# Performance work log

Measured on AMD Instinct MI355X. Metric: run time of the kernel, lower is better.

## Reference

```python
import jax, jax.numpy as jnp
import numpy as np

D_PROJ = 256
SCALE = D_PROJ ** (-0.5)


def setup_inputs() -> dict:
    key = jax.random.key(0)
    k1, k2, k3, k4 = jax.random.split(key, 4)
    B, L, Dh = 16, 2048, 1280
    T, Dg = 512, 768
    H = jax.random.normal(k1, (B, L, Dh), dtype=jnp.float32)
    G = jax.random.normal(k2, (B, T, Dg), dtype=jnp.float32)
    # Linear weights (torch nn.Linear: out = x @ W.T), small init to keep softmax well-conditioned
    Wq = jax.random.normal(k3, (D_PROJ, Dg), dtype=jnp.float32) * 0.02
    Wk = jax.random.normal(k4, (D_PROJ, Dh), dtype=jnp.float32) * 0.02
    return {"H": H, "G": G, "Wq": Wq, "Wk": Wk}


def reference(H, G, Wq, Wk):
    # Q = Wq(G): [B,T,P]; K = Wk(H): [B,L,P]
    Q = jnp.einsum('btg,pg->btp', G, Wq)
    K = jnp.einsum('bld,pd->blp', H, Wk)
    # The torch module's chunked online-softmax computes exact softmax over L.
    logits = jnp.einsum('btp,blp->btl', Q, K) * SCALE  # [B,T,L]
    A = jax.nn.softmax(logits, axis=-1)
    # Values are the raw residue embeddings H (not projected).
    Z = jnp.einsum('btl,bld->btd', A, H)  # [B,T,Dh]
    return Z
```

## Files before the change

### kernel.cpp

```cpp
#include <hip/hip_runtime.h>
#include <stdint.h>

typedef __attribute__((ext_vector_type(8))) short   short8;
typedef __attribute__((ext_vector_type(8))) __bf16  bf16x8;
typedef __attribute__((ext_vector_type(4))) float   floatx4;

#define DEV static __device__ __forceinline__

DEV unsigned short f2b(float f) {
  union { float f; unsigned u; } v; v.f = f;
  unsigned u = v.u;
  unsigned r = u + 0x7FFFu + ((u >> 16) & 1u);
  return (unsigned short)(r >> 16);
}

DEV void gload_lds16(const void* g, void* l) {
  __builtin_amdgcn_global_load_lds(
      (const __attribute__((address_space(1))) unsigned int*)g,
      (__attribute__((address_space(3))) unsigned int*)l,
      16, 0, 0);
}

__global__ void cvtw_kernel(const float* __restrict__ a, unsigned short* __restrict__ oa, int na4,
                            const float* __restrict__ b, unsigned short* __restrict__ ob, int nb4,
                            float* __restrict__ zp, int nz) {
  int i = blockIdx.x * blockDim.x + threadIdx.x;
  if (i < na4) {
    float4 v = ((const float4*)a)[i];
    ushort4 o; o.x = f2b(v.x); o.y = f2b(v.y); o.z = f2b(v.z); o.w = f2b(v.w);
    ((ushort4*)oa)[i] = o;
  } else if (i < na4 + nb4) {
    int k = i - na4;
    float4 v = ((const float4*)b)[k];
    ushort4 o; o.x = f2b(v.x); o.y = f2b(v.y); o.z = f2b(v.z); o.w = f2b(v.w);
    ((ushort4*)ob)[k] = o;
  } else if (i < na4 + nb4 + nz) {
    zp[i - na4 - nb4] = 0.f;
  }
}

template <int WRITE_HT>
__global__ __launch_bounds__(256) void proj_gemm(
    const float* __restrict__ A32, const unsigned short* __restrict__ Bt,
    unsigned short* __restrict__ C, unsigned short* __restrict__ HT,
    int K, int lda) {
  __shared__ float          Af32[2][64 * 32];
  __shared__ unsigned short Bs[2][256 * 32];
  __shared__ unsigned short As[64 * 32];
  __shared__ unsigned short At2[WRITE_HT ? 32 * 66 : 1];

  const int m0   = blockIdx.x * 64;
  const int t    = threadIdx.x;
  const int lane = t & 63;
  const int wave = t >> 6;
  const int wn   = wave * 64;
  const int r16  = lane & 15;
  const int q    = lane >> 4;
  const int nt   = K >> 5;

  floatx4 acc[4][4];
#pragma unroll
  for (int i = 0; i < 4; ++i)
#pragma unroll
    for (int j = 0; j < 4; ++j) acc[i][j] = (floatx4){0.f, 0.f, 0.f, 0.f};

  auto stage = [&](int it, int buf) {
    const int kt = it << 5;
#pragma unroll
    for (int cc = 0; cc < 2; ++cc) {
      int c = t + cc * 256;
      gload_lds16(A32 + (size_t)(m0 + (c >> 3)) * lda + kt + (c & 7) * 4,
                  &Af32[buf][c * 4]);
    }
#pragma unroll
    for (int cc = 0; cc < 4; ++cc) {
      int c = t + cc * 256;
      gload_lds16(Bt + (size_t)(c >> 2) * K + kt + (c & 3) * 8, &Bs[buf][c * 8]);
    }
  };

  stage(0, 0);
  stage(1, 1);

  for (int it = 0; it < nt; ++it) {
    const int cur = it & 1;
    const int kt  = it << 5;

    if (it == nt - 1) { asm volatile("s_waitcnt vmcnt(0)" ::: "memory"); }
    else              { asm volatile("s_waitcnt vmcnt(6)" ::: "memory"); }
    __builtin_amdgcn_sched_barrier(0);

    {
      const int row = t >> 3;
      const int kc  = t & 7;
      float4 v0 = *(const float4*)&Af32[cur][t * 4];
      float4 v1 = *(const float4*)&Af32[cur][t * 4 + 1024];
      unsigned short e0[4], e1[4];
      e0[0] = f2b(v0.x); e0[1] = f2b(v0.y); e0[2] = f2b(v0.z); e0[3] = f2b(v0.w);
      e1[0] = f2b(v1.x); e1[1] = f2b(v1.y); e1[2] = f2b(v1.z); e1[3] = f2b(v1.w);
      ushort4 p0, p1;
      p0.x = e0[0]; p0.y = e0[1]; p0.z = e0[2]; p0.w = e0[3];
      p1.x = e1[0]; p1.y = e1[1]; p1.z = e1[2]; p1.w = e1[3];
      *(ushort4*)&As[row * 32 + kc * 4]        = p0;
      *(ushort4*)&As[(row + 32) * 32 + kc * 4] = p1;
      if constexpr (WRITE_HT) {
#pragma unroll
        for (int jj = 0; jj < 4; ++jj) {
          At2[(kc * 4 + jj) * 66 + row]      = e0[jj];
          At2[(kc * 4 + jj) * 66 + row + 32] = e1[jj];
        }
      }
    }
    asm volatile("s_waitcnt lgkmcnt(0)\n\ts_barrier" ::: "memory");
    __builtin_amdgcn_sched_barrier(0);

    bf16x8 af[4], bfr[4];
#pragma unroll
    for (int i = 0; i < 4; ++i) af[i]  = *(const bf16x8*)&As[(i * 16 + r16) * 32 + q * 8];
#pragma unroll
    for (int j = 0; j < 4; ++j) bfr[j] = *(const bf16x8*)&Bs[cur][(wn + j * 16 + r16) * 32 + q * 8];
    union { unsigned u[4]; short8 s; } vv;
    if constexpr (WRITE_HT) {
      const int d  = t >> 3;
      const int lc = t & 7;
      const unsigned* w = (const unsigned*)At2 + d * 33 + lc * 4;
      vv.u[0] = w[0]; vv.u[1] = w[1]; vv.u[2] = w[2]; vv.u[3] = w[3];
    }
    asm volatile("s_waitcnt lgkmcnt(0)\n\ts_barrier" ::: "memory");
    __builtin_amdgcn_sched_barrier(0);

    if (it + 2 < nt) stage(it + 2, cur);

#pragma unroll
    for (int i = 0; i < 4; ++i)
#pragma unroll
      for (int j = 0; j < 4; ++j)
        acc[i][j] = __builtin_amdgcn_mfma_f32_16x16x32_bf16(af[i], bfr[j], acc[i][j], 0, 0, 0);

    if constexpr (WRITE_HT) {
      const int d  = t >> 3;
      const int lc = t & 7;
      const int b  = m0 >> 11;
      const int l0 = m0 & 2047;
      *(short8*)&HT[((size_t)b * 1280 + kt + d) * 2048 + l0 + lc * 8] = vv.s;
    }
  }

#pragma unroll
  for (int i = 0; i < 4; ++i) {
#pragma unroll
    for (int r = 0; r < 4; ++r) {
      int m = m0 + i * 16 + q * 4 + r;
#pragma unroll
      for (int j = 0; j < 4; ++j) {
        int n = wn + j * 16 + r16;
        C[(size_t)m * 256 + n] = f2b(acc[i][j][r]);
      }
    }
  }
}

template <int EPI>
__global__ void gemm_nt(const unsigned short* __restrict__ Ab, const unsigned short* __restrict__ Btb,
                        void* __restrict__ Cpv, float* __restrict__ sums,
                        int K, int lda, int ldb, int ldc,
                        long long sA, long long sB, long long sC, int sstride,
                        float escale, int nx, int tiles_pb) {
  __shared__ unsigned short As[128 * 32];
  __shared__ unsigned short Bs[128 * 32];

  const int g   = blockIdx.x;
  const int xcd = g & 7;
  const int jj  = g >> 3;
  const int bz  = xcd * 2 + jj / tiles_pb;
  const int tt  = jj % tiles_pb;
  const int m0  = (tt / nx) * 128;
  const int n0  = (tt % nx) * 128;

  const int t    = threadIdx.x;
  const int lane = t & 63;
  const int wave = t >> 6;
  const int wm   = (wave & 1) * 64;
  const int wn   = (wave >> 1) * 64;
  const int r16  = lane & 15;
  const int q    = lane >> 4;

  const unsigned short* Bt = Btb + (long long)bz * sB;
  const unsigned short* A  = Ab + (long long)bz * sA;

  floatx4 acc[4][4];
#pragma unroll
  for (int i = 0; i < 4; ++i)
#pragma unroll
    for (int j = 0; j < 4; ++j) acc[i][j] = (floatx4){0.f, 0.f, 0.f, 0.f};

  for (int kt = 0; kt < K; kt += 32) {
    __syncthreads();
#pragma unroll
    for (int cc = 0; cc < 2; ++cc) {
      int c = t + cc * 256;
      gload_lds16(Bt + (size_t)(n0 + (c >> 2)) * ldb + kt + (c & 3) * 8, &Bs[c * 8]);
    }
#pragma unroll
    for (int cc = 0; cc < 2; ++cc) {
      int c = t + cc * 256;
      gload_lds16(A + (size_t)(m0 + (c >> 2)) * lda + kt + (c & 3) * 8, &As[c * 8]);
    }
    __syncthreads();

    bf16x8 af[4], bfr[4];
#pragma unroll
    for (int i = 0; i < 4; ++i) af[i]  = *(const bf16x8*)&As[(wm + i * 16 + r16) * 32 + q * 8];
#pragma unroll
    for (int j = 0; j < 4; ++j) bfr[j] = *(const bf16x8*)&Bs[(wn + j * 16 + r16) * 32 + q * 8];
#pragma unroll
    for (int i = 0; i < 4; ++i)
#pragma unroll
      for (int j = 0; j < 4; ++j)
        acc[i][j] = __builtin_amdgcn_mfma_f32_16x16x32_bf16(af[i], bfr[j], acc[i][j], 0, 0, 0);
  }

  if constexpr (EPI == 1) {
    unsigned short* C = (unsigned short*)Cpv + (long long)bz * sC;
#pragma unroll
    for (int i = 0; i < 4; ++i) {
#pragma unroll
      for (int r = 0; r < 4; ++r) {
        int m = m0 + wm + i * 16 + q * 4 + r;
        float ps = 0.f;
#pragma unroll
        for (int j = 0; j < 4; ++j) {
          int n = n0 + wn + j * 16 + r16;
          float v = __expf(acc[i][j][r] * escale);
          ps += v;
          C[(size_t)m * ldc + n] = f2b(v);
        }
#pragma unroll
        for (int msk = 1; msk < 16; msk <<= 1) ps += __shfl_xor(ps, msk, 64);
        if (r16 == 0) atomicAdd(&sums[(long long)bz * sstride + m], ps);
      }
    }
  } else {
    float* C = (float*)Cpv + (long long)bz * sC;
    const float* sb = sums + (long long)bz * sstride;
#pragma unroll
    for (int i = 0; i < 4; ++i) {
#pragma unroll
      for (int r = 0; r < 4; ++r) {
        int m = m0 + wm + i * 16 + q * 4 + r;
        float sc = 1.0f / sb[m];
#pragma unroll
        for (int j = 0; j < 4; ++j) {
          int n = n0 + wn + j * 16 + r16;
          C[(size_t)m * ldc + n] = acc[i][j][r] * sc;
        }
      }
    }
  }
}

extern "C" void kernel_launch(void* const* d_in, const int* in_sizes, int n_in,
                              void* d_out, int out_size, void* d_ws, size_t ws_size,
                              hipStream_t stream) {
  (void)in_sizes; (void)n_in; (void)out_size; (void)ws_size;
  const float* H  = (const float*)d_in[0];
  const float* G  = (const float*)d_in[1];
  const float* Wq = (const float*)d_in[2];
  const float* Wk = (const float*)d_in[3];
  float* Z = (float*)d_out;

  constexpr int B = 16, L = 2048, Dh = 1280, T = 512, Dg = 768, P = 256;

  char* ws = (char*)d_ws;
  size_t off = 0;
  auto alloc = [&](size_t bytes) { void* p = ws + off; off += (bytes + 255) & ~(size_t)255; return p; };
  unsigned short* Wqbf = (unsigned short*)alloc((size_t)P * Dg * 2);
  unsigned short* Wkbf = (unsigned short*)alloc((size_t)P * Dh * 2);
  unsigned short* Qbf  = (unsigned short*)alloc((size_t)B * T * P * 2);
  unsigned short* Kbf  = (unsigned short*)alloc((size_t)B * L * P * 2);
  unsigned short* HT   = (unsigned short*)alloc((size_t)B * Dh * L * 2);
  unsigned short* E    = (unsigned short*)alloc((size_t)B * T * L * 2);
  float*          sums = (float*)alloc((size_t)B * T * 4);

  {
    int na4 = P * Dg / 4, nb4 = P * Dh / 4, nz = B * T;
    cvtw_kernel<<<(na4 + nb4 + nz + 255) / 256, 256, 0, stream>>>(
        Wq, Wqbf, na4, Wk, Wkbf, nb4, sums, nz);
  }

  proj_gemm<0><<<B * T / 64, 256, 0, stream>>>(G, Wqbf, Qbf, nullptr, Dg, Dg);
  proj_gemm<1><<<B * L / 64, 256, 0, stream>>>(H, Wkbf, Kbf, HT, Dh, Dh);

  gemm_nt<1><<<B * (T / 128) * (L / 128), 256, 0, stream>>>(
      Qbf, Kbf, E, sums, P, P, P, L,
      (long long)T * P, (long long)L * P, (long long)T * L, T,
      0.0625f, L / 128, (T / 128) * (L / 128));

  gemm_nt<2><<<B * (T / 128) * (Dh / 128), 256, 0, stream>>>(
      E, HT, Z, sums, L, L, L, Dh,
      (long long)T * L, (long long)Dh * L, (long long)T * Dh, T,
      0.f, Dh / 128, (T / 128) * (Dh / 128));
}
```

Baseline: 410.9 us.

## Add dedicated 128-row K projection kernel with register-staged fp32 loads

Replaces the templated K projection, which also writes the bf16 transpose of H, with a new proj_k kernel using 128-row tiles and 512 threads (2x4 wave grid). The fp32 H tile is now loaded into registers and converted there instead of being staged through LDS with global_load_lds. The loop is unrolled by two with explicit vmcnt bookkeeping, and each staged W tile is shared by twice as many rows. This is meant to cut LDS traffic and per-row weight reloads in the largest projection, at the cost of more registers and a bigger block.

```diff
diff --git a/kernel.cpp b/kernel.cpp
--- a/kernel.cpp
+++ b/kernel.cpp
@@ -47,7 +47,6 @@
   __shared__ float          Af32[2][64 * 32];
   __shared__ unsigned short Bs[2][256 * 32];
   __shared__ unsigned short As[64 * 32];
-  __shared__ unsigned short At2[WRITE_HT ? 32 * 66 : 1];
 
   const int m0   = blockIdx.x * 64;
   const int t    = threadIdx.x;
@@ -84,7 +83,6 @@
 
   for (int it = 0; it < nt; ++it) {
     const int cur = it & 1;
-    const int kt  = it << 5;
 
     if (it == nt - 1) { asm volatile("s_waitcnt vmcnt(0)" ::: "memory"); }
     else              { asm volatile("s_waitcnt vmcnt(6)" ::: "memory"); }
@@ -95,21 +93,11 @@
       const int kc  = t & 7;
       float4 v0 = *(const float4*)&Af32[cur][t * 4];
       float4 v1 = *(const float4*)&Af32[cur][t * 4 + 1024];
-      unsigned short e0[4], e1[4];
-      e0[0] = f2b(v0.x); e0[1] = f2b(v0.y); e0[2] = f2b(v0.z); e0[3] = f2b(v0.w);
-      e1[0] = f2b(v1.x); e1[1] = f2b(v1.y); e1[2] = f2b(v1.z); e1[3] = f2b(v1.w);
       ushort4 p0, p1;
-      p0.x = e0[0]; p0.y = e0[1]; p0.z = e0[2]; p0.w = e0[3];
-      p1.x = e1[0]; p1.y = e1[1]; p1.z = e1[2]; p1.w = e1[3];
+      p0.x = f2b(v0.x); p0.y = f2b(v0.y); p0.z = f2b(v0.z); p0.w = f2b(v0.w);
+      p1.x = f2b(v1.x); p1.y = f2b(v1.y); p1.z = f2b(v1.z); p1.w = f2b(v1.w);
       *(ushort4*)&As[row * 32 + kc * 4]        = p0;
       *(ushort4*)&As[(row + 32) * 32 + kc * 4] = p1;
-      if constexpr (WRITE_HT) {
-#pragma unroll
-        for (int jj = 0; jj < 4; ++jj) {
-          At2[(kc * 4 + jj) * 66 + row]      = e0[jj];
-          At2[(kc * 4 + jj) * 66 + row + 32] = e1[jj];
-        }
-      }
     }
     asm volatile("s_waitcnt lgkmcnt(0)\n\ts_barrier" ::: "memory");
     __builtin_amdgcn_sched_barrier(0);
@@ -119,13 +107,6 @@
     for (int i = 0; i < 4; ++i) af[i]  = *(const bf16x8*)&As[(i * 16 + r16) * 32 + q * 8];
 #pragma unroll
     for (int j = 0; j < 4; ++j) bfr[j] = *(const bf16x8*)&Bs[cur][(wn + j * 16 + r16) * 32 + q * 8];
-    union { unsigned u[4]; short8 s; } vv;
-    if constexpr (WRITE_HT) {
-      const int d  = t >> 3;
-      const int lc = t & 7;
-      const unsigned* w = (const unsigned*)At2 + d * 33 + lc * 4;
-      vv.u[0] = w[0]; vv.u[1] = w[1]; vv.u[2] = w[2]; vv.u[3] = w[3];
-    }
     asm volatile("s_waitcnt lgkmcnt(0)\n\ts_barrier" ::: "memory");
     __builtin_amdgcn_sched_barrier(0);
 
@@ -136,14 +117,6 @@
 #pragma unroll
       for (int j = 0; j < 4; ++j)
         acc[i][j] = __builtin_amdgcn_mfma_f32_16x16x32_bf16(af[i], bfr[j], acc[i][j], 0, 0, 0);
-
-    if constexpr (WRITE_HT) {
-      const int d  = t >> 3;
-      const int lc = t & 7;
-      const int b  = m0 >> 11;
-      const int l0 = m0 & 2047;
-      *(short8*)&HT[((size_t)b * 1280 + kt + d) * 2048 + l0 + lc * 8] = vv.s;
-    }
   }
 
 #pragma unroll
@@ -151,6 +124,144 @@
 #pragma unroll
     for (int r = 0; r < 4; ++r) {
       int m = m0 + i * 16 + q * 4 + r;
+#pragma unroll
+      for (int j = 0; j < 4; ++j) {
+        int n = wn + j * 16 + r16;
+        C[(size_t)m * 256 + n] = f2b(acc[i][j][r]);
+      }
+    }
+  }
+}
+
+DEV void projk_step(int it, int nt, float4 (&VA)[2],
+                    unsigned short* __restrict__ BsBuf,
+                    unsigned short* __restrict__ As,
+                    unsigned short* __restrict__ At2,
+                    const unsigned short* __restrict__ Bt,
+                    unsigned short* __restrict__ HT,
+                    const float* __restrict__ ag,
+                    int K, int t, int wm, int wn, int r16, int q,
+                    int arow, int aseg, int d, int lc,
+                    size_t ht_base, floatx4 (&acc)[4][4]) {
+  const int kt = it << 5;
+  if (it == 0)            asm volatile("s_waitcnt vmcnt(4)" ::: "memory");
+  else if (it == 1)       asm volatile("s_waitcnt vmcnt(5)" ::: "memory");
+  else if (it == nt - 1)  asm volatile("s_waitcnt vmcnt(2)" ::: "memory");
+  else                    asm volatile("s_waitcnt vmcnt(6)" ::: "memory");
+  __builtin_amdgcn_sched_barrier(0);
+
+  unsigned short e0 = f2b(VA[0].x), e1 = f2b(VA[0].y), e2 = f2b(VA[0].z), e3 = f2b(VA[0].w);
+  unsigned short e4 = f2b(VA[1].x), e5 = f2b(VA[1].y), e6 = f2b(VA[1].z), e7 = f2b(VA[1].w);
+  short8 pk;
+  pk[0] = (short)e0; pk[1] = (short)e1; pk[2] = (short)e2; pk[3] = (short)e3;
+  pk[4] = (short)e4; pk[5] = (short)e5; pk[6] = (short)e6; pk[7] = (short)e7;
+  *(short8*)&As[arow * 32 + aseg * 8] = pk;
+  const int kb = aseg * 8;
+  At2[(kb + 0) * 130 + arow] = e0;
+  At2[(kb + 1) * 130 + arow] = e1;
+  At2[(kb + 2) * 130 + arow] = e2;
+  At2[(kb + 3) * 130 + arow] = e3;
+  At2[(kb + 4) * 130 + arow] = e4;
+  At2[(kb + 5) * 130 + arow] = e5;
+  At2[(kb + 6) * 130 + arow] = e6;
+  At2[(kb + 7) * 130 + arow] = e7;
+  asm volatile("s_waitcnt lgkmcnt(0)\n\ts_barrier" ::: "memory");
+  __builtin_amdgcn_sched_barrier(0);
+
+  bf16x8 af[4], bfr[4];
+#pragma unroll
+  for (int i = 0; i < 4; ++i) af[i]  = *(const bf16x8*)&As[(wm + i * 16 + r16) * 32 + q * 8];
+#pragma unroll
+  for (int j = 0; j < 4; ++j) bfr[j] = *(const bf16x8*)&BsBuf[(wn + j * 16 + r16) * 32 + q * 8];
+  union { unsigned u[4]; short8 s; } vv;
+  {
+    const unsigned* w = (const unsigned*)At2 + d * 65 + lc * 4;
+    vv.u[0] = w[0]; vv.u[1] = w[1]; vv.u[2] = w[2]; vv.u[3] = w[3];
+  }
+  asm volatile("s_waitcnt lgkmcnt(0)\n\ts_barrier" ::: "memory");
+  __builtin_amdgcn_sched_barrier(0);
+
+  if (it + 2 < nt) {
+    const int kt2 = (it + 2) << 5;
+#pragma unroll
+    for (int cc = 0; cc < 2; ++cc) {
+      int c = t + cc * 512;
+      gload_lds16(Bt + (size_t)(c >> 2) * K + kt2 + (c & 3) * 8, &BsBuf[c * 8]);
+    }
+    VA[0] = *(const float4*)(ag + (size_t)(it + 2) * 32);
+    VA[1] = *(const float4*)(ag + (size_t)(it + 2) * 32 + 4);
+  }
+  __builtin_amdgcn_sched_barrier(0);
+
+#pragma unroll
+  for (int i = 0; i < 4; ++i)
+#pragma unroll
+    for (int j = 0; j < 4; ++j)
+      acc[i][j] = __builtin_amdgcn_mfma_f32_16x16x32_bf16(af[i], bfr[j], acc[i][j], 0, 0, 0);
+
+  *(short8*)&HT[ht_base + (size_t)kt * 2048] = vv.s;
+}
+
+__global__ __launch_bounds__(512) void proj_k(
+    const float* __restrict__ A32, const unsigned short* __restrict__ Bt,
+    unsigned short* __restrict__ C, unsigned short* __restrict__ HT,
+    int K, int lda) {
+  __shared__ unsigned short Bs[2][256 * 32];
+  __shared__ unsigned short As[128 * 32];
+  __shared__ unsigned short At2[32 * 130];
+
+  const int m0   = blockIdx.x * 128;
+  const int t    = threadIdx.x;
+  const int lane = t & 63;
+  const int wave = t >> 6;
+  const int wm   = (wave & 1) * 64;
+  const int wn   = (wave >> 1) * 64;
+  const int r16  = lane & 15;
+  const int q    = lane >> 4;
+  const int nt   = K >> 5;
+
+  const int arow = t >> 2;
+  const int aseg = t & 3;
+  const float* ag = A32 + (size_t)(m0 + arow) * lda + aseg * 8;
+
+  const int d  = t >> 4;
+  const int lc = t & 15;
+  const size_t ht_base = ((size_t)(m0 >> 11) * 1280 + d) * 2048 + (m0 & 2047) + lc * 8;
+
+  floatx4 acc[4][4];
+#pragma unroll
+  for (int i = 0; i < 4; ++i)
+#pragma unroll
+    for (int j = 0; j < 4; ++j) acc[i][j] = (floatx4){0.f, 0.f, 0.f, 0.f};
+
+  float4 va0[2], va1[2];
+#pragma unroll
+  for (int cc = 0; cc < 2; ++cc) {
+    int c = t + cc * 512;
+    gload_lds16(Bt + (size_t)(c >> 2) * K + (c & 3) * 8, &Bs[0][c * 8]);
+  }
+  va0[0] = *(const float4*)(ag);
+  va0[1] = *(const float4*)(ag + 4);
+#pragma unroll
+  for (int cc = 0; cc < 2; ++cc) {
+    int c = t + cc * 512;
+    gload_lds16(Bt + (size_t)(c >> 2) * K + 32 + (c & 3) * 8, &Bs[1][c * 8]);
+  }
+  va1[0] = *(const float4*)(ag + 32);
+  va1[1] = *(const float4*)(ag + 36);
+
+  for (int it2 = 0; it2 < nt; it2 += 2) {
+    projk_step(it2,     nt, va0, Bs[0], As, At2, Bt, HT, ag, K, t, wm, wn, r16, q,
+               arow, aseg, d, lc, ht_base, acc);
+    projk_step(it2 + 1, nt, va1, Bs[1], As, At2, Bt, HT, ag, K, t, wm, wn, r16, q,
+               arow, aseg, d, lc, ht_base, acc);
+  }
+
+#pragma unroll
+  for (int i = 0; i < 4; ++i) {
+#pragma unroll
+    for (int r = 0; r < 4; ++r) {
+      int m = m0 + wm + i * 16 + q * 4 + r;
 #pragma unroll
       for (int j = 0; j < 4; ++j) {
         int n = wn + j * 16 + r16;
@@ -289,7 +400,7 @@
   }
 
   proj_gemm<0><<<B * T / 64, 256, 0, stream>>>(G, Wqbf, Qbf, nullptr, Dg, Dg);
-  proj_gemm<1><<<B * L / 64, 256, 0, stream>>>(H, Wkbf, Kbf, HT, Dh, Dh);
+  proj_k<<<B * L / 128, 512, 0, stream>>>(H, Wkbf, Kbf, HT, Dh, Dh);
 
   gemm_nt<1><<<B * (T / 128) * (L / 128), 256, 0, stream>>>(
       Qbf, Kbf, E, sums, P, P, P, L,
```

Result: no change. 415.8 us (+1.2%).

## Shrink projection M-tile, register-prefetch fp32 A, and double-buffer batched GEMM

Applied to the files above, without the earlier changes.

The projection GEMM moves from 64-row to 32-row tiles. Its fp32 A operand is now prefetched straight into registers instead of being staged through LDS, with an unrolled two-step loop and hand-tuned vmcnt waits that count both the LDS-direct B loads and the register A loads. The batched gemm_nt kernel gains double-buffered LDS so the next K-tile loads while the current one computes, which removes one barrier per iteration. The aim is more blocks for occupancy and better latency hiding, at the cost of more B-tile reloads per output row and fragile manual waitcnt bookkeeping.

```diff
diff --git a/kernel.cpp b/kernel.cpp
--- a/kernel.cpp
+++ b/kernel.cpp
@@ -40,16 +40,86 @@
 }
 
 template <int WRITE_HT>
-__global__ __launch_bounds__(256) void proj_gemm(
+DEV void proj32_step(int it, int nt, float4& VA,
+                     unsigned short* __restrict__ BsBuf,
+                     unsigned short* __restrict__ As,
+                     unsigned short* __restrict__ At2,
+                     const unsigned short* __restrict__ Bt,
+                     unsigned short* __restrict__ HT,
+                     const float* __restrict__ ag,
+                     int K, int t, int wn, int r16, int q,
+                     int arow, int aseg, int d, int lc,
+                     size_t ht_base, floatx4 (&acc)[2][4]) {
+  const int kt = it << 5;
+  if constexpr (WRITE_HT) {
+    if (it == 0)            asm volatile("s_waitcnt vmcnt(5)" ::: "memory");
+    else if (it == 1)       asm volatile("s_waitcnt vmcnt(6)" ::: "memory");
+    else if (it == nt - 1)  asm volatile("s_waitcnt vmcnt(2)" ::: "memory");
+    else                    asm volatile("s_waitcnt vmcnt(7)" ::: "memory");
+  } else {
+    if (it == nt - 1)       asm volatile("s_waitcnt vmcnt(0)" ::: "memory");
+    else                    asm volatile("s_waitcnt vmcnt(5)" ::: "memory");
+  }
+  __builtin_amdgcn_sched_barrier(0);
+
+  unsigned short e0 = f2b(VA.x), e1 = f2b(VA.y), e2 = f2b(VA.z), e3 = f2b(VA.w);
+  ushort4 pk; pk.x = e0; pk.y = e1; pk.z = e2; pk.w = e3;
+  *(ushort4*)&As[arow * 32 + aseg * 4] = pk;
+  if constexpr (WRITE_HT) {
+    const int kb = aseg * 4;
+    At2[(kb + 0) * 66 + arow] = e0;
+    At2[(kb + 1) * 66 + arow] = e1;
+    At2[(kb + 2) * 66 + arow] = e2;
+    At2[(kb + 3) * 66 + arow] = e3;
+  }
+  asm volatile("s_waitcnt lgkmcnt(0)\n\ts_barrier" ::: "memory");
+  __builtin_amdgcn_sched_barrier(0);
+
+  bf16x8 af[2], bfr[4];
+#pragma unroll
+  for (int i = 0; i < 2; ++i) af[i]  = *(const bf16x8*)&As[(i * 16 + r16) * 32 + q * 8];
+#pragma unroll
+  for (int j = 0; j < 4; ++j) bfr[j] = *(const bf16x8*)&BsBuf[(wn + j * 16 + r16) * 32 + q * 8];
+  union { unsigned u[2]; ushort4 s; } vv;
+  if constexpr (WRITE_HT) {
+    const unsigned* w = (const unsigned*)At2 + d * 33 + lc * 2;
+    vv.u[0] = w[0]; vv.u[1] = w[1];
+  }
+  asm volatile("s_waitcnt lgkmcnt(0)\n\ts_barrier" ::: "memory");
+  __builtin_amdgcn_sched_barrier(0);
+
+  if (it + 2 < nt) {
+    const int kt2 = (it + 2) << 5;
+#pragma unroll
+    for (int cc = 0; cc < 4; ++cc) {
+      int c = t + cc * 256;
+      gload_lds16(Bt + (size_t)(c >> 2) * K + kt2 + (c & 3) * 8, &BsBuf[c * 8]);
+    }
+    VA = *(const float4*)(ag + (size_t)(it + 2) * 32);
+  }
+  __builtin_amdgcn_sched_barrier(0);
+
+#pragma unroll
+  for (int i = 0; i < 2; ++i)
+#pragma unroll
+    for (int j = 0; j < 4; ++j)
+      acc[i][j] = __builtin_amdgcn_mfma_f32_16x16x32_bf16(af[i], bfr[j], acc[i][j], 0, 0, 0);
+
+  if constexpr (WRITE_HT) {
+    *(ushort4*)&HT[ht_base + (size_t)kt * 2048] = vv.s;
+  }
+}
+
+template <int WRITE_HT>
+__global__ __launch_bounds__(256) void proj32(
     const float* __restrict__ A32, const unsigned short* __restrict__ Bt,
     unsigned short* __restrict__ C, unsigned short* __restrict__ HT,
     int K, int lda) {
-  __shared__ float          Af32[2][64 * 32];
   __shared__ unsigned short Bs[2][256 * 32];
-  __shared__ unsigned short As[64 * 32];
+  __shared__ unsigned short As[32 * 32];
   __shared__ unsigned short At2[WRITE_HT ? 32 * 66 : 1];
 
-  const int m0   = blockIdx.x * 64;
+  const int m0   = blockIdx.x * 32;
   const int t    = threadIdx.x;
   const int lane = t & 63;
   const int wave = t >> 6;
@@ -58,96 +128,43 @@
   const int q    = lane >> 4;
   const int nt   = K >> 5;
 
-  floatx4 acc[4][4];
-#pragma unroll
-  for (int i = 0; i < 4; ++i)
+  const int arow = t >> 3;
+  const int aseg = t & 7;
+  const float* ag = A32 + (size_t)(m0 + arow) * lda + aseg * 4;
+
+  const int d  = t >> 3;
+  const int lc = t & 7;
+  const size_t ht_base = ((size_t)(m0 >> 11) * 1280 + d) * 2048 + (m0 & 2047) + lc * 4;
+
+  floatx4 acc[2][4];
+#pragma unroll
+  for (int i = 0; i < 2; ++i)
 #pragma unroll
     for (int j = 0; j < 4; ++j) acc[i][j] = (floatx4){0.f, 0.f, 0.f, 0.f};
 
-  auto stage = [&](int it, int buf) {
-    const int kt = it << 5;
-#pragma unroll
-    for (int cc = 0; cc < 2; ++cc) {
-      int c = t + cc * 256;
-      gload_lds16(A32 + (size_t)(m0 + (c >> 3)) * lda + kt + (c & 7) * 4,
-                  &Af32[buf][c * 4]);
-    }
-#pragma unroll
-    for (int cc = 0; cc < 4; ++cc) {
-      int c = t + cc * 256;
-      gload_lds16(Bt + (size_t)(c >> 2) * K + kt + (c & 3) * 8, &Bs[buf][c * 8]);
-    }
-  };
-
-  stage(0, 0);
-  stage(1, 1);
-
-  for (int it = 0; it < nt; ++it) {
-    const int cur = it & 1;
-    const int kt  = it << 5;
-
-    if (it == nt - 1) { asm volatile("s_waitcnt vmcnt(0)" ::: "memory"); }
-    else              { asm volatile("s_waitcnt vmcnt(6)" ::: "memory"); }
-    __builtin_amdgcn_sched_barrier(0);
-
-    {
-      const int row = t >> 3;
-      const int kc  = t & 7;
-      float4 v0 = *(const float4*)&Af32[cur][t * 4];
-      float4 v1 = *(const float4*)&Af32[cur][t * 4 + 1024];
-      unsigned short e0[4], e1[4];
-      e0[0] = f2b(v0.x); e0[1] = f2b(v0.y); e0[2] = f2b(v0.z); e0[3] = f2b(v0.w);
-      e1[0] = f2b(v1.x); e1[1] = f2b(v1.y); e1[2] = f2b(v1.z); e1[3] = f2b(v1.w);
-      ushort4 p0, p1;
-      p0.x = e0[0]; p0.y = e0[1]; p0.z = e0[2]; p0.w = e0[3];
-      p1.x = e1[0]; p1.y = e1[1]; p1.z = e1[2]; p1.w = e1[3];
-      *(ushort4*)&As[row * 32 + kc * 4]        = p0;
-      *(ushort4*)&As[(row + 32) * 32 + kc * 4] = p1;
-      if constexpr (WRITE_HT) {
-#pragma unroll
-        for (int jj = 0; jj < 4; ++jj) {
-          At2[(kc * 4 + jj) * 66 + row]      = e0[jj];
-          At2[(kc * 4 + jj) * 66 + row + 32] = e1[jj];
-        }
-      }
-    }
-    asm volatile("s_waitcnt lgkmcnt(0)\n\ts_barrier" ::: "memory");
-    __builtin_amdgcn_sched_barrier(0);
-
-    bf16x8 af[4], bfr[4];
-#pragma unroll
-    for (int i = 0; i < 4; ++i) af[i]  = *(const bf16x8*)&As[(i * 16 + r16) * 32 + q * 8];
-#pragma unroll
-    for (int j = 0; j < 4; ++j) bfr[j] = *(const bf16x8*)&Bs[cur][(wn + j * 16 + r16) * 32 + q * 8];
-    union { unsigned u[4]; short8 s; } vv;
-    if constexpr (WRITE_HT) {
-      const int d  = t >> 3;
-      const int lc = t & 7;
-      const unsigned* w = (const unsigned*)At2 + d * 33 + lc * 4;
-      vv.u[0] = w[0]; vv.u[1] = w[1]; vv.u[2] = w[2]; vv.u[3] = w[3];
-    }
-    asm volatile("s_waitcnt lgkmcnt(0)\n\ts_barrier" ::: "memory");
-    __builtin_amdgcn_sched_barrier(0);
-
-    if (it + 2 < nt) stage(it + 2, cur);
-
-#pragma unroll
-    for (int i = 0; i < 4; ++i)
-#pragma unroll
-      for (int j = 0; j < 4; ++j)
-        acc[i][j] = __builtin_amdgcn_mfma_f32_16x16x32_bf16(af[i], bfr[j], acc[i][j], 0, 0, 0);
-
-    if constexpr (WRITE_HT) {
-      const int d  = t >> 3;
-      const int lc = t & 7;
-      const int b  = m0 >> 11;
-      const int l0 = m0 & 2047;
-      *(short8*)&HT[((size_t)b * 1280 + kt + d) * 2048 + l0 + lc * 8] = vv.s;
-    }
-  }
-
-#pragma unroll
-  for (int i = 0; i < 4; ++i) {
+  float4 va0, va1;
+#pragma unroll
+  for (int cc = 0; cc < 4; ++cc) {
+    int c = t + cc * 256;
+    gload_lds16(Bt + (size_t)(c >> 2) * K + (c & 3) * 8, &Bs[0][c * 8]);
+  }
+  va0 = *(const float4*)(ag);
+#pragma unroll
+  for (int cc = 0; cc < 4; ++cc) {
+    int c = t + cc * 256;
+    gload_lds16(Bt + (size_t)(c >> 2) * K + 32 + (c & 3) * 8, &Bs[1][c * 8]);
+  }
+  va1 = *(const float4*)(ag + 32);
+
+  for (int it2 = 0; it2 < nt; it2 += 2) {
+    proj32_step<WRITE_HT>(it2,     nt, va0, Bs[0], As, At2, Bt, HT, ag, K,
+                          t, wn, r16, q, arow, aseg, d, lc, ht_base, acc);
+    proj32_step<WRITE_HT>(it2 + 1, nt, va1, Bs[1], As, At2, Bt, HT, ag, K,
+                          t, wn, r16, q, arow, aseg, d, lc, ht_base, acc);
+  }
+
+#pragma unroll
+  for (int i = 0; i < 2; ++i) {
 #pragma unroll
     for (int r = 0; r < 4; ++r) {
       int m = m0 + i * 16 + q * 4 + r;
@@ -166,8 +183,8 @@
                         int K, int lda, int ldb, int ldc,
                         long long sA, long long sB, long long sC, int sstride,
                         float escale, int nx, int tiles_pb) {
-  __shared__ unsigned short As[128 * 32];
-  __shared__ unsigned short Bs[128 * 32];
+  __shared__ unsigned short As[2][128 * 32];
+  __shared__ unsigned short Bs[2][128 * 32];
 
   const int g   = blockIdx.x;
   const int xcd = g & 7;
@@ -184,6 +201,7 @@
   const int wn   = (wave >> 1) * 64;
   const int r16  = lane & 15;
   const int q    = lane >> 4;
+  const int nt   = K >> 5;
 
   const unsigned short* Bt = Btb + (long long)bz * sB;
   const unsigned short* A  = Ab + (long long)bz * sA;
@@ -194,30 +212,40 @@
 #pragma unroll
     for (int j = 0; j < 4; ++j) acc[i][j] = (floatx4){0.f, 0.f, 0.f, 0.f};
 
-  for (int kt = 0; kt < K; kt += 32) {
-    __syncthreads();
+  auto stage = [&](int it, int buf) {
+    const int kt = it << 5;
 #pragma unroll
     for (int cc = 0; cc < 2; ++cc) {
       int c = t + cc * 256;
-      gload_lds16(Bt + (size_t)(n0 + (c >> 2)) * ldb + kt + (c & 3) * 8, &Bs[c * 8]);
+      gload_lds16(Bt + (size_t)(n0 + (c >> 2)) * ldb + kt + (c & 3) * 8, &Bs[buf][c * 8]);
     }
 #pragma unroll
     for (int cc = 0; cc < 2; ++cc) {
       int c = t + cc * 256;
-      gload_lds16(A + (size_t)(m0 + (c >> 2)) * lda + kt + (c & 3) * 8, &As[c * 8]);
-    }
-    __syncthreads();
+      gload_lds16(A + (size_t)(m0 + (c >> 2)) * lda + kt + (c & 3) * 8, &As[buf][c * 8]);
+    }
+  };
+
+  stage(0, 0);
+  __syncthreads();
+
+  for (int it = 0; it < nt; ++it) {
+    const int cur = it & 1;
+
+    if (it + 1 < nt) stage(it + 1, cur ^ 1);
 
     bf16x8 af[4], bfr[4];
 #pragma unroll
-    for (int i = 0; i < 4; ++i) af[i]  = *(const bf16x8*)&As[(wm + i * 16 + r16) * 32 + q * 8];
-#pragma unroll
-    for (int j = 0; j < 4; ++j) bfr[j] = *(const bf16x8*)&Bs[(wn + j * 16 + r16) * 32 + q * 8];
+    for (int i = 0; i < 4; ++i) af[i]  = *(const bf16x8*)&As[cur][(wm + i * 16 + r16) * 32 + q * 8];
+#pragma unroll
+    for (int j = 0; j < 4; ++j) bfr[j] = *(const bf16x8*)&Bs[cur][(wn + j * 16 + r16) * 32 + q * 8];
 #pragma unroll
     for (int i = 0; i < 4; ++i)
 #pragma unroll
       for (int j = 0; j < 4; ++j)
         acc[i][j] = __builtin_amdgcn_mfma_f32_16x16x32_bf16(af[i], bfr[j], acc[i][j], 0, 0, 0);
+
+    __syncthreads();
   }
 
   if constexpr (EPI == 1) {
@@ -288,8 +316,8 @@
         Wq, Wqbf, na4, Wk, Wkbf, nb4, sums, nz);
   }
 
-  proj_gemm<0><<<B * T / 64, 256, 0, stream>>>(G, Wqbf, Qbf, nullptr, Dg, Dg);
-  proj_gemm<1><<<B * L / 64, 256, 0, stream>>>(H, Wkbf, Kbf, HT, Dh, Dh);
+  proj32<0><<<B * T / 32, 256, 0, stream>>>(G, Wqbf, Qbf, nullptr, Dg, Dg);
+  proj32<1><<<B * L / 32, 256, 0, stream>>>(H, Wkbf, Kbf, HT, Dh, Dh);
 
   gemm_nt<1><<<B * (T / 128) * (L / 128), 256, 0, stream>>>(
       Qbf, Kbf, E, sums, P, P, P, L,
```

Measured after the change: 472.7 us. 15.1% more time.

## Drop transposed bf16 H copy; read fp32 H directly in PV GEMM with double buffering

Applied to the files above, without the earlier changes.

Removes the HT transposed bf16 buffer that the K projection wrote. The final A·H GEMM becomes a new NN kernel that loads fp32 H rows, converts them to bf16 and writes them transposed into padded LDS. The QK GEMM also gains double-buffered LDS staging so global loads overlap the MFMAs. This saves writing and re-reading an 84MB intermediate, but the PV GEMM now reads fp32 H (twice the bytes per tile), converts it in registers, and does scattered 2-byte LDS stores.

```diff
diff --git a/kernel.cpp b/kernel.cpp
--- a/kernel.cpp
+++ b/kernel.cpp
@@ -47,7 +47,6 @@
   __shared__ float          Af32[2][64 * 32];
   __shared__ unsigned short Bs[2][256 * 32];
   __shared__ unsigned short As[64 * 32];
-  __shared__ unsigned short At2[WRITE_HT ? 32 * 66 : 1];
 
   const int m0   = blockIdx.x * 64;
   const int t    = threadIdx.x;
@@ -84,7 +83,6 @@
 
   for (int it = 0; it < nt; ++it) {
     const int cur = it & 1;
-    const int kt  = it << 5;
 
     if (it == nt - 1) { asm volatile("s_waitcnt vmcnt(0)" ::: "memory"); }
     else              { asm volatile("s_waitcnt vmcnt(6)" ::: "memory"); }
@@ -95,21 +93,11 @@
       const int kc  = t & 7;
       float4 v0 = *(const float4*)&Af32[cur][t * 4];
       float4 v1 = *(const float4*)&Af32[cur][t * 4 + 1024];
-      unsigned short e0[4], e1[4];
-      e0[0] = f2b(v0.x); e0[1] = f2b(v0.y); e0[2] = f2b(v0.z); e0[3] = f2b(v0.w);
-      e1[0] = f2b(v1.x); e1[1] = f2b(v1.y); e1[2] = f2b(v1.z); e1[3] = f2b(v1.w);
       ushort4 p0, p1;
-      p0.x = e0[0]; p0.y = e0[1]; p0.z = e0[2]; p0.w = e0[3];
-      p1.x = e1[0]; p1.y = e1[1]; p1.z = e1[2]; p1.w = e1[3];
+      p0.x = f2b(v0.x); p0.y = f2b(v0.y); p0.z = f2b(v0.z); p0.w = f2b(v0.w);
+      p1.x = f2b(v1.x); p1.y = f2b(v1.y); p1.z = f2b(v1.z); p1.w = f2b(v1.w);
       *(ushort4*)&As[row * 32 + kc * 4]        = p0;
       *(ushort4*)&As[(row + 32) * 32 + kc * 4] = p1;
-      if constexpr (WRITE_HT) {
-#pragma unroll
-        for (int jj = 0; jj < 4; ++jj) {
-          At2[(kc * 4 + jj) * 66 + row]      = e0[jj];
-          At2[(kc * 4 + jj) * 66 + row + 32] = e1[jj];
-        }
-      }
     }
     asm volatile("s_waitcnt lgkmcnt(0)\n\ts_barrier" ::: "memory");
     __builtin_amdgcn_sched_barrier(0);
@@ -119,13 +107,6 @@
     for (int i = 0; i < 4; ++i) af[i]  = *(const bf16x8*)&As[(i * 16 + r16) * 32 + q * 8];
 #pragma unroll
     for (int j = 0; j < 4; ++j) bfr[j] = *(const bf16x8*)&Bs[cur][(wn + j * 16 + r16) * 32 + q * 8];
-    union { unsigned u[4]; short8 s; } vv;
-    if constexpr (WRITE_HT) {
-      const int d  = t >> 3;
-      const int lc = t & 7;
-      const unsigned* w = (const unsigned*)At2 + d * 33 + lc * 4;
-      vv.u[0] = w[0]; vv.u[1] = w[1]; vv.u[2] = w[2]; vv.u[3] = w[3];
-    }
     asm volatile("s_waitcnt lgkmcnt(0)\n\ts_barrier" ::: "memory");
     __builtin_amdgcn_sched_barrier(0);
 
@@ -136,14 +117,6 @@
 #pragma unroll
       for (int j = 0; j < 4; ++j)
         acc[i][j] = __builtin_amdgcn_mfma_f32_16x16x32_bf16(af[i], bfr[j], acc[i][j], 0, 0, 0);
-
-    if constexpr (WRITE_HT) {
-      const int d  = t >> 3;
-      const int lc = t & 7;
-      const int b  = m0 >> 11;
-      const int l0 = m0 & 2047;
-      *(short8*)&HT[((size_t)b * 1280 + kt + d) * 2048 + l0 + lc * 8] = vv.s;
-    }
   }
 
 #pragma unroll
@@ -166,8 +139,8 @@
                         int K, int lda, int ldb, int ldc,
                         long long sA, long long sB, long long sC, int sstride,
                         float escale, int nx, int tiles_pb) {
-  __shared__ unsigned short As[128 * 32];
-  __shared__ unsigned short Bs[128 * 32];
+  __shared__ unsigned short As[2][128 * 32];
+  __shared__ unsigned short Bs[2][128 * 32];
 
   const int g   = blockIdx.x;
   const int xcd = g & 7;
@@ -184,6 +157,7 @@
   const int wn   = (wave >> 1) * 64;
   const int r16  = lane & 15;
   const int q    = lane >> 4;
+  const int nt   = K >> 5;
 
   const unsigned short* Bt = Btb + (long long)bz * sB;
   const unsigned short* A  = Ab + (long long)bz * sA;
@@ -194,30 +168,40 @@
 #pragma unroll
     for (int j = 0; j < 4; ++j) acc[i][j] = (floatx4){0.f, 0.f, 0.f, 0.f};
 
-  for (int kt = 0; kt < K; kt += 32) {
-    __syncthreads();
+  auto stage = [&](int it, int buf) {
+    const int kt = it << 5;
 #pragma unroll
     for (int cc = 0; cc < 2; ++cc) {
       int c = t + cc * 256;
-      gload_lds16(Bt + (size_t)(n0 + (c >> 2)) * ldb + kt + (c & 3) * 8, &Bs[c * 8]);
+      gload_lds16(Bt + (size_t)(n0 + (c >> 2)) * ldb + kt + (c & 3) * 8, &Bs[buf][c * 8]);
     }
 #pragma unroll
     for (int cc = 0; cc < 2; ++cc) {
       int c = t + cc * 256;
-      gload_lds16(A + (size_t)(m0 + (c >> 2)) * lda + kt + (c & 3) * 8, &As[c * 8]);
-    }
-    __syncthreads();
+      gload_lds16(A + (size_t)(m0 + (c >> 2)) * lda + kt + (c & 3) * 8, &As[buf][c * 8]);
+    }
+  };
+
+  stage(0, 0);
+  __syncthreads();
+
+  for (int it = 0; it < nt; ++it) {
+    const int cur = it & 1;
+
+    if (it + 1 < nt) stage(it + 1, cur ^ 1);
 
     bf16x8 af[4], bfr[4];
 #pragma unroll
-    for (int i = 0; i < 4; ++i) af[i]  = *(const bf16x8*)&As[(wm + i * 16 + r16) * 32 + q * 8];
-#pragma unroll
-    for (int j = 0; j < 4; ++j) bfr[j] = *(const bf16x8*)&Bs[(wn + j * 16 + r16) * 32 + q * 8];
+    for (int i = 0; i < 4; ++i) af[i]  = *(const bf16x8*)&As[cur][(wm + i * 16 + r16) * 32 + q * 8];
+#pragma unroll
+    for (int j = 0; j < 4; ++j) bfr[j] = *(const bf16x8*)&Bs[cur][(wn + j * 16 + r16) * 32 + q * 8];
 #pragma unroll
     for (int i = 0; i < 4; ++i)
 #pragma unroll
       for (int j = 0; j < 4; ++j)
         acc[i][j] = __builtin_amdgcn_mfma_f32_16x16x32_bf16(af[i], bfr[j], acc[i][j], 0, 0, 0);
+
+    __syncthreads();
   }
 
   if constexpr (EPI == 1) {
@@ -240,20 +224,118 @@
         if (r16 == 0) atomicAdd(&sums[(long long)bz * sstride + m], ps);
       }
     }
-  } else {
-    float* C = (float*)Cpv + (long long)bz * sC;
-    const float* sb = sums + (long long)bz * sstride;
-#pragma unroll
-    for (int i = 0; i < 4; ++i) {
-#pragma unroll
-      for (int r = 0; r < 4; ++r) {
-        int m = m0 + wm + i * 16 + q * 4 + r;
-        float sc = 1.0f / sb[m];
-#pragma unroll
-        for (int j = 0; j < 4; ++j) {
-          int n = n0 + wn + j * 16 + r16;
-          C[(size_t)m * ldc + n] = acc[i][j][r] * sc;
-        }
+  }
+}
+
+__global__ void gemm_nn(const unsigned short* __restrict__ Ab, const float* __restrict__ Hb,
+                        float* __restrict__ Cp, const float* __restrict__ sums,
+                        int K, int lda, int ldb, int ldc,
+                        long long sA, long long sB, long long sC, int sstride,
+                        int nx, int tiles_pb) {
+  constexpr int BP = 40;
+  __shared__ unsigned short As[2][128 * 32];
+  __shared__ unsigned short Bsn[2][128 * BP];
+
+  const int g   = blockIdx.x;
+  const int xcd = g & 7;
+  const int jj  = g >> 3;
+  const int bz  = xcd * 2 + jj / tiles_pb;
+  const int tt  = jj % tiles_pb;
+  const int m0  = (tt / nx) * 128;
+  const int n0  = (tt % nx) * 128;
+
+  const int t    = threadIdx.x;
+  const int lane = t & 63;
+  const int wave = t >> 6;
+  const int wm   = (wave & 1) * 64;
+  const int wn   = (wave >> 1) * 64;
+  const int r16  = lane & 15;
+  const int q    = lane >> 4;
+  const int nt   = K >> 5;
+
+  const unsigned short* A = Ab + (long long)bz * sA;
+  const float*          H = Hb + (long long)bz * sB;
+
+  const int kr  = t >> 3;
+  const int nc0 = (t & 7) * 16;
+
+  floatx4 acc[4][4];
+#pragma unroll
+  for (int i = 0; i < 4; ++i)
+#pragma unroll
+    for (int j = 0; j < 4; ++j) acc[i][j] = (floatx4){0.f, 0.f, 0.f, 0.f};
+
+  auto stageA = [&](int it, int buf) {
+    const int kt = it << 5;
+#pragma unroll
+    for (int cc = 0; cc < 2; ++cc) {
+      int c = t + cc * 256;
+      gload_lds16(A + (size_t)(m0 + (c >> 2)) * lda + kt + (c & 3) * 8, &As[buf][c * 8]);
+    }
+  };
+  auto loadB = [&](int it, float4 (&h)[4]) {
+    const float* hp = H + (size_t)((it << 5) + kr) * ldb + n0 + nc0;
+    h[0] = ((const float4*)hp)[0];
+    h[1] = ((const float4*)hp)[1];
+    h[2] = ((const float4*)hp)[2];
+    h[3] = ((const float4*)hp)[3];
+  };
+  auto writeB = [&](int buf, const float4 (&h)[4]) {
+    unsigned short* bp = &Bsn[buf][0];
+#pragma unroll
+    for (int v4 = 0; v4 < 4; ++v4) {
+      bp[(nc0 + v4 * 4 + 0) * BP + kr] = f2b(h[v4].x);
+      bp[(nc0 + v4 * 4 + 1) * BP + kr] = f2b(h[v4].y);
+      bp[(nc0 + v4 * 4 + 2) * BP + kr] = f2b(h[v4].z);
+      bp[(nc0 + v4 * 4 + 3) * BP + kr] = f2b(h[v4].w);
+    }
+  };
+
+  {
+    float4 h[4];
+    stageA(0, 0);
+    loadB(0, h);
+    writeB(0, h);
+  }
+  __syncthreads();
+
+  for (int it = 0; it < nt; ++it) {
+    const int cur = it & 1;
+
+    float4 h[4];
+    if (it + 1 < nt) {
+      stageA(it + 1, cur ^ 1);
+      loadB(it + 1, h);
+    }
+
+    bf16x8 af[4], bfr[4];
+#pragma unroll
+    for (int i = 0; i < 4; ++i) af[i]  = *(const bf16x8*)&As[cur][(wm + i * 16 + r16) * 32 + q * 8];
+#pragma unroll
+    for (int j = 0; j < 4; ++j) bfr[j] = *(const bf16x8*)&Bsn[cur][(wn + j * 16 + r16) * BP + q * 8];
+#pragma unroll
+    for (int i = 0; i < 4; ++i)
+#pragma unroll
+      for (int j = 0; j < 4; ++j)
+        acc[i][j] = __builtin_amdgcn_mfma_f32_16x16x32_bf16(af[i], bfr[j], acc[i][j], 0, 0, 0);
+
+    if (it + 1 < nt) writeB(cur ^ 1, h);
+
+    __syncthreads();
+  }
+
+  float* C = Cp + (long long)bz * sC;
+  const float* sb = sums + (long long)bz * sstride;
+#pragma unroll
+  for (int i = 0; i < 4; ++i) {
+#pragma unroll
+    for (int r = 0; r < 4; ++r) {
+      int m = m0 + wm + i * 16 + q * 4 + r;
+      float sc = 1.0f / sb[m];
+#pragma unroll
+      for (int j = 0; j < 4; ++j) {
+        int n = n0 + wn + j * 16 + r16;
+        C[(size_t)m * ldc + n] = acc[i][j][r] * sc;
       }
     }
   }
@@ -278,7 +360,6 @@
   unsigned short* Wkbf = (unsigned short*)alloc((size_t)P * Dh * 2);
   unsigned short* Qbf  = (unsigned short*)alloc((size_t)B * T * P * 2);
   unsigned short* Kbf  = (unsigned short*)alloc((size_t)B * L * P * 2);
-  unsigned short* HT   = (unsigned short*)alloc((size_t)B * Dh * L * 2);
   unsigned short* E    = (unsigned short*)alloc((size_t)B * T * L * 2);
   float*          sums = (float*)alloc((size_t)B * T * 4);
 
@@ -289,15 +370,15 @@
   }
 
   proj_gemm<0><<<B * T / 64, 256, 0, stream>>>(G, Wqbf, Qbf, nullptr, Dg, Dg);
-  proj_gemm<1><<<B * L / 64, 256, 0, stream>>>(H, Wkbf, Kbf, HT, Dh, Dh);
+  proj_gemm<0><<<B * L / 64, 256, 0, stream>>>(H, Wkbf, Kbf, nullptr, Dh, Dh);
 
   gemm_nt<1><<<B * (T / 128) * (L / 128), 256, 0, stream>>>(
       Qbf, Kbf, E, sums, P, P, P, L,
       (long long)T * P, (long long)L * P, (long long)T * L, T,
       0.0625f, L / 128, (T / 128) * (L / 128));
 
-  gemm_nt<2><<<B * (T / 128) * (Dh / 128), 256, 0, stream>>>(
-      E, HT, Z, sums, L, L, L, Dh,
-      (long long)T * L, (long long)Dh * L, (long long)T * Dh, T,
-      0.f, Dh / 128, (T / 128) * (Dh / 128));
-}
+  gemm_nn<<<B * (T / 128) * (Dh / 128), 256, 0, stream>>>(
+      E, H, Z, sums, L, L, Dh, Dh,
+      (long long)T * L, (long long)L * Dh, (long long)T * Dh, T,
+      Dh / 128, (T / 128) * (Dh / 128));
+}
```

Result: slower. 464.4 us (+13.0%).
